# Kernel optimization log

Hardware: AMD Instinct MI355X
Metric: run time of the kernel (lower is better)

Reference implementation:

```python
import jax, jax.numpy as jnp
import numpy as np


def setup_inputs() -> dict:
    key = jax.random.key(0)
    ks = jax.random.split(key, 9)
    b, t_q, t_k, n_q, n_k = 4, 128, 512, 512, 512
    out_size = 512
    s = 0.02  # small init scale for weights
    return {
        "query": jax.random.normal(ks[0], (b, t_q, n_q), jnp.float32),
        "keys": jax.random.normal(ks[1], (b, t_k, n_k), jnp.float32),
        "values": jax.random.normal(ks[2], (b, t_k, n_k), jnp.float32),
        "W_q": jax.random.normal(ks[3], (n_k, n_q), jnp.float32) * s,
        "b_q": jnp.zeros((n_k,), jnp.float32),
        "w_att": jax.random.normal(ks[4], (n_k,), jnp.float32) * s,
        "b_att": jnp.zeros((1,), jnp.float32),
        "W_out": jax.random.normal(ks[5], (out_size, n_q + n_k), jnp.float32) * s,
        "b_out": jnp.zeros((out_size,), jnp.float32),
    }


def reference(query, keys, values, W_q, b_q, w_att, b_att, W_out, b_out):
    # linear_q: [b, t_q, query_size] -> [b, t_q, key_size]
    att_query = jnp.einsum("bqd,nd->bqn", query, W_q) + b_q
    # Bahdanau additive score: tanh(q + k) projected by linear_att (key_size -> 1)
    # intermediate: [b, t_q, t_k, n]
    sum_qk = jnp.tanh(att_query[:, :, None, :] + keys[:, None, :, :])
    scores = jnp.einsum("bqkn,n->bqk", sum_qk, w_att) + b_att[0]
    # mask is None by default; dropout p=0 -> identity
    probs = jax.nn.softmax(scores, axis=-1)  # [b, t_q, t_k]
    context = jnp.einsum("bqk,bkn->bqn", probs, values)
    # linear_out on concat([query, context]) + tanh nonlinearity
    cat = jnp.concatenate([query, context], axis=-1)
    out = jnp.tanh(jnp.einsum("bqc,oc->bqo", cat, W_out) + b_out)
    return out, probs
```

## Files before the change

### kernel.cpp

```cpp
#include <hip/hip_runtime.h>
#include <hip/hip_fp16.h>


#define BB    4
#define TQ    128
#define TK    512
#define NN    512
#define OUTSZ 512
#define CATSZ 1024
#define K2E   2.8853900817779268f
#define L2E   1.4426950408889634f
#define MAT   262144
#define WS_HALVES (11 * MAT)

typedef __attribute__((ext_vector_type(4))) _Float16 half4;
typedef __attribute__((ext_vector_type(2))) _Float16 h2;

#if __has_builtin(__builtin_amdgcn_exp2f)
#define EXP2F(x) __builtin_amdgcn_exp2f(x)
#else
#define EXP2F(x) exp2f(x)
#endif
#if __has_builtin(__builtin_amdgcn_rcpf)
#define RCPF(x) __builtin_amdgcn_rcpf(x)
#else
#define RCPF(x) (1.0f / (x))
#endif

__device__ __forceinline__ h2 u2h(unsigned int u) {
  union { unsigned int i; h2 h; } v; v.i = u; return v.h;
}
#if __has_builtin(__builtin_amdgcn_fdot2)
__device__ __forceinline__ float FDOT2(h2 a, h2 b, float c) {
  return __builtin_amdgcn_fdot2(a, b, c, false);
}
#else
__device__ __forceinline__ float FDOT2(h2 a, h2 b, float c) {
  return fmaf((float)a.x, (float)b.x, fmaf((float)a.y, (float)b.y, c));
}
#endif

__device__ __forceinline__ float fast_tanh(float x) {
  float e = EXP2F(x * K2E);
  return fmaf(-2.0f, RCPF(e + 1.0f), 1.0f);
}
__device__ __forceinline__ float waveRedSum(float s) {
  #pragma unroll
  for (int m = 32; m >= 1; m >>= 1) s += __shfl_xor(s, m, 64);
  return s;
}
__device__ __forceinline__ float waveRedMax(float s) {
  #pragma unroll
  for (int m = 32; m >= 1; m >>= 1) s = fmaxf(s, __shfl_xor(s, m, 64));
  return s;
}
__device__ __forceinline__ float fma4(float4 w, float4 v, float acc) {
  acc = fmaf(w.x, v.x, acc); acc = fmaf(w.y, v.y, acc);
  acc = fmaf(w.z, v.z, acc); acc = fmaf(w.w, v.w, acc);
  return acc;
}
__device__ __forceinline__ float4 scqh(float4 s, half4 E, float A, float w) {
  s.x = fmaf(w, RCPF(fmaf((float)E.x, A, 1.0f)), s.x);
  s.y = fmaf(w, RCPF(fmaf((float)E.y, A, 1.0f)), s.y);
  s.z = fmaf(w, RCPF(fmaf((float)E.z, A, 1.0f)), s.z);
  s.w = fmaf(w, RCPF(fmaf((float)E.w, A, 1.0f)), s.w);
  return s;
}
__device__ __forceinline__ void dotq(float4& r0, float4& r1, uint4 wp, uint2 cp) {
  h2 c0 = u2h(cp.x), c1 = u2h(cp.y);
  r0.x = FDOT2(u2h(wp.x), c0, r0.x); r1.x = FDOT2(u2h(wp.x), c1, r1.x);
  r0.y = FDOT2(u2h(wp.y), c0, r0.y); r1.y = FDOT2(u2h(wp.y), c1, r1.y);
  r0.z = FDOT2(u2h(wp.z), c0, r0.z); r1.z = FDOT2(u2h(wp.z), c1, r1.z);
  r0.w = FDOT2(u2h(wp.w), c0, r0.w); r1.w = FDOT2(u2h(wp.w), c1, r1.w);
}

__global__ __launch_bounds__(256)
void pack_kernel(const float* __restrict__ keys, const float* __restrict__ W_q,
                 const float* __restrict__ W_out, const float* __restrict__ values,
                 _Float16* __restrict__ ws)
{
  __shared__ float tile[32][33];
  const int idx = blockIdx.x;
  const int tx = threadIdx.x & 31, ty = threadIdx.x >> 5;

  if (idx >= 1792) {
    int r = idx - 1792;
    int b = r >> 8, k2 = r & 255;
    const float* r0 = values + ((size_t)b * 512 + 2 * k2) * 512;
    const float* r1 = r0 + 512;
    int n0 = threadIdx.x * 2;
    float2 a = *(const float2*)(r0 + n0);
    float2 c = *(const float2*)(r1 + n0);
    _Float16* dst = ws + (size_t)7 * MAT + (size_t)b * MAT + k2 * 1024 + n0 * 2;
    half4 h = {(_Float16)a.x, (_Float16)c.x, (_Float16)a.y, (_Float16)c.y};
    *(half4*)dst = h;
    return;
  }

  if (idx < 1024) {
    int b = idx >> 8, r = idx & 255;
    int by = r >> 4, bx = r & 15;
    const float* src = keys + (size_t)b * MAT;
    _Float16* dst = ws + (size_t)b * MAT;
    #pragma unroll
    for (int i = 0; i < 32; i += 8)
      tile[ty + i][tx] = src[(size_t)(by * 32 + ty + i) * 512 + bx * 32 + tx] * K2E;
    __syncthreads();
    #pragma unroll
    for (int i = 0; i < 32; i += 8)
      dst[(size_t)(bx * 32 + ty + i) * 512 + by * 32 + tx] = (_Float16)EXP2F(tile[tx][ty + i]);
    return;
  }

  const float* src; _Float16* dst; int N; int by, bx;
  if (idx < 1280) {
    int r = idx - 1024; by = r >> 4; bx = r & 15;
    src = W_q; dst = ws + (size_t)4 * MAT; N = 512;
  } else {
    int r = idx - 1280; by = r >> 5; bx = r & 31;
    src = W_out; dst = ws + (size_t)5 * MAT; N = 1024;
  }
  #pragma unroll
  for (int i = 0; i < 32; i += 8)
    tile[ty + i][tx] = src[(size_t)(by * 32 + ty + i) * N + bx * 32 + tx];
  __syncthreads();
  #pragma unroll
  for (int i = 0; i < 32; i += 8) {
    int d = bx * 32 + ty + i;
    int o = by * 32 + tx;
    dst[(size_t)(d >> 1) * 1024 + o * 2 + (d & 1)] = (_Float16)tile[tx][ty + i];
  }
}

__global__ __launch_bounds__(1024, 4)
void attn_main(const float* __restrict__ query,
               const float* __restrict__ b_q, const float* __restrict__ w_att,
               const float* __restrict__ b_att, const float* __restrict__ b_out,
               const _Float16* __restrict__ ws,
               float* __restrict__ out, float* __restrict__ probs)
{
  __shared__ __align__(16) _Float16 catH[2048];
  __shared__ __align__(16) float4 paw[NN];
  __shared__ __align__(16) _Float16 prH[1024];
  __shared__ __align__(16) float  pt[8][2][NN];
  __shared__ float redm[2][8], reds2[2][8], redw[8];

  const _Float16* wsKeys  = ws;
  const _Float16* wsWqP   = ws + (size_t)4 * MAT;
  const _Float16* wsWoutP = ws + (size_t)5 * MAT;
  const _Float16* wsValP  = ws + (size_t)7 * MAT;

  const int t    = threadIdx.x;
  const int qh   = t >> 9;
  const int u    = t & 511;
  const int G    = t >> 7;
  const int v    = t & 127;
  const int wave = t >> 6, lane = t & 63, wq8 = wave & 7;

  const int p  = blockIdx.x;
  const int b  = (p & 7) >> 1;
  const int qg = ((p >> 3) << 1) | (p & 1);
  const int qabs0 = qg * 2;

  const float batt = b_att[0];

  float w_own = 0.f;
  if (qh == 0) {
    float q0 = query[((size_t)(b * TQ + qabs0 + 0)) * NN + u];
    float q1 = query[((size_t)(b * TQ + qabs0 + 1)) * NN + u];
    catH[(u >> 1) * 4 + (u & 1)]     = (_Float16)q0;
    catH[(u >> 1) * 4 + 2 + (u & 1)] = (_Float16)q1;
  } else {
    w_own = w_att[u];
  }
  if (qh == 1) {
    float wp = waveRedSum(w_own);
    if (lane == 0) redw[wq8] = wp;
  }
  __syncthreads();
  const float sumW = redw[0]+redw[1]+redw[2]+redw[3]+redw[4]+redw[5]+redw[6]+redw[7];

  {
    const _Float16* wq = wsWqP + 8 * v;
    float4 a0 = {0,0,0,0}, a1 = {0,0,0,0};
    #pragma unroll 4
    for (int j2 = 0; j2 < 32; ++j2) {
      int d2 = 32 * G + j2;
      uint4 wp = *(const uint4*)(wq + (size_t)d2 * 1024);
      uint2 cp = *(const uint2*)(&catH[d2 * 4]);
      dotq(a0, a1, wp, cp);
    }
    *(float4*)(&pt[G][0][4 * v]) = a0;
    *(float4*)(&pt[G][1][4 * v]) = a1;
  }
  __syncthreads();
  {
    float s = pt[0][qh][u] + pt[1][qh][u] + pt[2][qh][u] + pt[3][qh][u]
            + pt[4][qh][u] + pt[5][qh][u] + pt[6][qh][u] + pt[7][qh][u];
    float A = EXP2F(K2E * (s + b_q[u]));
    if (qh == 0) { paw[u].x = A; paw[u].z = w_att[u]; }
    else         { paw[u].y = A; }
  }
  __syncthreads();

  {
    const _Float16* ke = wsKeys + (size_t)b * MAT + 4 * v;
    float4 s0 = {0,0,0,0}, s1 = {0,0,0,0};
    #pragma unroll 8
    for (int j = 0; j < 64; ++j) {
      int n = 64 * G + j;
      half4 E   = *(const half4*)(ke + (size_t)n * 512);
      float4 pw = paw[n];
      s0 = scqh(s0, E, pw.x, pw.z);
      s1 = scqh(s1, E, pw.y, pw.z);
    }
    *(float4*)(&pt[G][0][4 * v]) = s0;
    *(float4*)(&pt[G][1][4 * v]) = s1;
  }
  __syncthreads();

  {
    float s = pt[0][qh][u] + pt[1][qh][u] + pt[2][qh][u] + pt[3][qh][u]
            + pt[4][qh][u] + pt[5][qh][u] + pt[6][qh][u] + pt[7][qh][u];
    float sc = batt + sumW - 2.0f * s;
    float m = waveRedMax(sc);
    if (lane == 0) redm[qh][wq8] = m;
    __syncthreads();
    float bm = fmaxf(fmaxf(fmaxf(redm[qh][0],redm[qh][1]),fmaxf(redm[qh][2],redm[qh][3])),
                     fmaxf(fmaxf(redm[qh][4],redm[qh][5]),fmaxf(redm[qh][6],redm[qh][7])));
    float e = EXP2F((sc - bm) * L2E);
    float se = waveRedSum(e);
    if (lane == 0) reds2[qh][wq8] = se;
    __syncthreads();
    float bs = reds2[qh][0]+reds2[qh][1]+reds2[qh][2]+reds2[qh][3]
             + reds2[qh][4]+reds2[qh][5]+reds2[qh][6]+reds2[qh][7];
    float pv = e * RCPF(bs);
    prH[(u >> 1) * 4 + qh * 2 + (u & 1)] = (_Float16)pv;
    probs[((size_t)(b * TQ + qabs0 + qh)) * TK + u] = pv;
  }
  __syncthreads();

  {
    const _Float16* vp = wsValP + (size_t)b * MAT + 8 * v;
    float4 c0 = {0,0,0,0}, c1 = {0,0,0,0};
    #pragma unroll 4
    for (int j2 = 0; j2 < 32; ++j2) {
      int k2 = 32 * G + j2;
      uint4 vk = *(const uint4*)(vp + (size_t)k2 * 1024);
      uint2 pp = *(const uint2*)(&prH[k2 * 4]);
      dotq(c0, c1, vk, pp);
    }
    *(float4*)(&pt[G][0][4 * v]) = c0;
    *(float4*)(&pt[G][1][4 * v]) = c1;
  }
  __syncthreads();
  {
    float s = pt[0][qh][u] + pt[1][qh][u] + pt[2][qh][u] + pt[3][qh][u]
            + pt[4][qh][u] + pt[5][qh][u] + pt[6][qh][u] + pt[7][qh][u];
    catH[(256 + (u >> 1)) * 4 + qh * 2 + (u & 1)] = (_Float16)s;
  }
  __syncthreads();

  {
    const _Float16* wo = wsWoutP + 8 * v;
    float4 o0 = {0,0,0,0}, o1 = {0,0,0,0};
    #pragma unroll 4
    for (int j2 = 0; j2 < 64; ++j2) {
      int c2 = 64 * G + j2;
      uint4 wp = *(const uint4*)(wo + (size_t)c2 * 1024);
      uint2 cp = *(const uint2*)(&catH[c2 * 4]);
      dotq(o0, o1, wp, cp);
    }
    *(float4*)(&pt[G][0][4 * v]) = o0;
    *(float4*)(&pt[G][1][4 * v]) = o1;
  }
  __syncthreads();
  {
    float s = pt[0][qh][u] + pt[1][qh][u] + pt[2][qh][u] + pt[3][qh][u]
            + pt[4][qh][u] + pt[5][qh][u] + pt[6][qh][u] + pt[7][qh][u];
    float oo = s + b_out[u];
    out[((size_t)(b * TQ + qabs0 + qh)) * OUTSZ + u] = fast_tanh(oo);
  }
}

__device__ __forceinline__ float sc4f(float4 w, float4 k, float4 a, float acc) {
  acc = fmaf(w.x, RCPF(EXP2F(fmaf(k.x, K2E, a.x)) + 1.0f), acc);
  acc = fmaf(w.y, RCPF(EXP2F(fmaf(k.y, K2E, a.y)) + 1.0f), acc);
  acc = fmaf(w.z, RCPF(EXP2F(fmaf(k.z, K2E, a.z)) + 1.0f), acc);
  acc = fmaf(w.w, RCPF(EXP2F(fmaf(k.w, K2E, a.w)) + 1.0f), acc);
  return acc;
}

__global__ __launch_bounds__(1024, 4)
void attn_fallback(const float* __restrict__ query, const float* __restrict__ keys,
                   const float* __restrict__ values, const float* __restrict__ W_q,
                   const float* __restrict__ b_q, const float* __restrict__ w_att,
                   const float* __restrict__ b_att, const float* __restrict__ W_out,
                   const float* __restrict__ b_out,
                   float* __restrict__ out, float* __restrict__ probs)
{
  __shared__ __align__(16) float qv[2][NN];
  __shared__ __align__(16) float aqc[2][NN];
  __shared__ __align__(16) float wv[NN];
  __shared__ __align__(16) float pr[2][TK];
  __shared__ __align__(16) float ctx[2][NN];
  __shared__ __align__(16) float part[2][2][NN];
  __shared__ float redm[2][8], reds[2][8], redw[8];

  const int t = threadIdx.x, H = t >> 9, u = t & 511;
  const int wave = t >> 6, lane = t & 63, wq8 = wave & 7;
  const int p = blockIdx.x, b = (p & 7) >> 1;
  const int qg = ((p >> 3) << 1) | (p & 1), qabs0 = qg * 2;
  const float batt = b_att[0];

  if (H == 0) wv[u] = w_att[u];
  qv[H][u] = query[((size_t)(b * TQ + qabs0 + H)) * NN + u];
  __syncthreads();
  if (H == 0) {
    float wp = waveRedSum(wv[u]);
    if (lane == 0) redw[wq8] = wp;
  }
  __syncthreads();
  const float sumW = redw[0]+redw[1]+redw[2]+redw[3]+redw[4]+redw[5]+redw[6]+redw[7];

  {
    const float4* wq4 = (const float4*)(W_q + (size_t)u * NN + 256 * H);
    const float4* x4  = (const float4*)(qv[0] + 256 * H);
    const float4* y4  = (const float4*)(qv[1] + 256 * H);
    float a0=0.f, a0b=0.f, a1=0.f, a1b=0.f;
    #pragma unroll 2
    for (int c = 0; c < 16; ++c) {
      float4 wA=wq4[4*c+0], wB=wq4[4*c+1], wC=wq4[4*c+2], wD=wq4[4*c+3];
      float4 xA=x4[4*c+0], xB=x4[4*c+1], xC=x4[4*c+2], xD=x4[4*c+3];
      a0 = fma4(wA,xA,a0); a0b = fma4(wB,xB,a0b);
      a0 = fma4(wC,xC,a0); a0b = fma4(wD,xD,a0b);
      float4 yA=y4[4*c+0], yB=y4[4*c+1], yC=y4[4*c+2], yD=y4[4*c+3];
      a1 = fma4(wA,yA,a1); a1b = fma4(wB,yB,a1b);
      a1 = fma4(wC,yC,a1); a1b = fma4(wD,yD,a1b);
    }
    part[H][0][u] = a0 + a0b; part[H][1][u] = a1 + a1b;
  }
  __syncthreads();
  aqc[H][u] = (part[0][H][u] + part[1][H][u] + b_q[u]) * K2E;
  __syncthreads();

  {
    const float4* kr  = (const float4*)(keys + ((size_t)(b * TK) + u) * NN + 256 * H);
    const float4* a0p = (const float4*)(aqc[0] + 256 * H);
    const float4* a1p = (const float4*)(aqc[1] + 256 * H);
    const float4* w4  = (const float4*)(wv + 256 * H);
    float s0 = 0.f, s1 = 0.f;
    #pragma unroll 2
    for (int c = 0; c < 16; ++c) {
      float4 kA=kr[4*c+0], kB=kr[4*c+1], kC=kr[4*c+2], kD=kr[4*c+3];
      float4 wA=w4[4*c+0], wB=w4[4*c+1], wC=w4[4*c+2], wD=w4[4*c+3];
      float4 aA=a0p[4*c+0], aB=a0p[4*c+1], aC=a0p[4*c+2], aD=a0p[4*c+3];
      s0 = sc4f(wA,kA,aA,s0); s0 = sc4f(wB,kB,aB,s0);
      s0 = sc4f(wC,kC,aC,s0); s0 = sc4f(wD,kD,aD,s0);
      float4 bA=a1p[4*c+0], bB=a1p[4*c+1], bC=a1p[4*c+2], bD=a1p[4*c+3];
      s1 = sc4f(wA,kA,bA,s1); s1 = sc4f(wB,kB,bB,s1);
      s1 = sc4f(wC,kC,bC,s1); s1 = sc4f(wD,kD,bD,s1);
    }
    part[H][0][u] = s0; part[H][1][u] = s1;
  }
  __syncthreads();

  {
    float sc = batt + sumW - 2.0f * (part[0][H][u] + part[1][H][u]);
    float m = waveRedMax(sc);
    if (lane == 0) redm[H][wq8] = m;
    __syncthreads();
    float bm = fmaxf(fmaxf(fmaxf(redm[H][0],redm[H][1]),fmaxf(redm[H][2],redm[H][3])),
                     fmaxf(fmaxf(redm[H][4],redm[H][5]),fmaxf(redm[H][6],redm[H][7])));
    float e = EXP2F((sc - bm) * L2E);
    float se = waveRedSum(e);
    if (lane == 0) reds[H][wq8] = se;
    __syncthreads();
    float bs = reds[H][0]+reds[H][1]+reds[H][2]+reds[H][3]
             + reds[H][4]+reds[H][5]+reds[H][6]+reds[H][7];
    float pv = e * RCPF(bs);
    pr[H][u] = pv;
    probs[((size_t)(b * TQ + qabs0 + H)) * TK + u] = pv;
  }
  __syncthreads();

  {
    const float* vcol = values + ((size_t)(b * TK) + 256 * H) * NN + u;
    const float4* p0 = (const float4*)(pr[0] + 256 * H);
    const float4* p1 = (const float4*)(pr[1] + 256 * H);
    float c0a=0.f, c0b=0.f, c1a=0.f, c1b=0.f;
    #pragma unroll 2
    for (int k = 0; k < 256; k += 8) {
      float v0 = vcol[(size_t)(k+0)*NN]; float v1 = vcol[(size_t)(k+1)*NN];
      float v2 = vcol[(size_t)(k+2)*NN]; float v3 = vcol[(size_t)(k+3)*NN];
      float v4 = vcol[(size_t)(k+4)*NN]; float v5 = vcol[(size_t)(k+5)*NN];
      float v6 = vcol[(size_t)(k+6)*NN]; float v7 = vcol[(size_t)(k+7)*NN];
      float4 pA = p0[k>>2], pB = p0[(k>>2)+1];
      float4 qA = p1[k>>2], qB = p1[(k>>2)+1];
      c0a = fmaf(pA.x,v0,c0a); c0a = fmaf(pA.y,v1,c0a);
      c0b = fmaf(pA.z,v2,c0b); c0b = fmaf(pA.w,v3,c0b);
      c0a = fmaf(pB.x,v4,c0a); c0a = fmaf(pB.y,v5,c0a);
      c0b = fmaf(pB.z,v6,c0b); c0b = fmaf(pB.w,v7,c0b);
      c1a = fmaf(qA.x,v0,c1a); c1a = fmaf(qA.y,v1,c1a);
      c1b = fmaf(qA.z,v2,c1b); c1b = fmaf(qA.w,v3,c1b);
      c1a = fmaf(qB.x,v4,c1a); c1a = fmaf(qB.y,v5,c1a);
      c1b = fmaf(qB.z,v6,c1b); c1b = fmaf(qB.w,v7,c1b);
    }
    part[H][0][u] = c0a + c0b; part[H][1][u] = c1a + c1b;
  }
  __syncthreads();
  ctx[H][u] = part[0][H][u] + part[1][H][u];
  __syncthreads();

  {
    const float4* wo = (const float4*)(W_out + (size_t)u * CATSZ + 512 * H);
    const float4* x4 = (H == 0) ? (const float4*)qv[0] : (const float4*)ctx[0];
    const float4* y4 = (H == 0) ? (const float4*)qv[1] : (const float4*)ctx[1];
    float o0=0.f, o0b=0.f, o1=0.f, o1b=0.f;
    #pragma unroll 2
    for (int c = 0; c < 32; ++c) {
      float4 wA=wo[4*c+0], wB=wo[4*c+1], wC=wo[4*c+2], wD=wo[4*c+3];
      float4 xA=x4[4*c+0], xB=x4[4*c+1], xC=x4[4*c+2], xD=x4[4*c+3];
      o0 = fma4(wA,xA,o0); o0b = fma4(wB,xB,o0b);
      o0 = fma4(wC,xC,o0); o0b = fma4(wD,xD,o0b);
      float4 yA=y4[4*c+0], yB=y4[4*c+1], yC=y4[4*c+2], yD=y4[4*c+3];
      o1 = fma4(wA,yA,o1); o1b = fma4(wB,yB,o1b);
      o1 = fma4(wC,yC,o1); o1b = fma4(wD,yD,o1b);
    }
    part[H][0][u] = o0 + o0b; part[H][1][u] = o1 + o1b;
  }
  __syncthreads();
  {
    float oo = part[0][H][u] + part[1][H][u] + b_out[u];
    out[((size_t)(b * TQ + qabs0 + H)) * OUTSZ + u] = fast_tanh(oo);
  }
}

extern "C" void kernel_launch(void* const* d_in, const int* in_sizes, int n_in,
                              void* d_out, int out_size, void* d_ws, size_t ws_size,
                              hipStream_t stream) {
  const float* query = (const float*)d_in[0];
  const float* keys  = (const float*)d_in[1];
  const float* vals  = (const float*)d_in[2];
  const float* W_q   = (const float*)d_in[3];
  const float* b_q   = (const float*)d_in[4];
  const float* w_att = (const float*)d_in[5];
  const float* b_att = (const float*)d_in[6];
  const float* W_out = (const float*)d_in[7];
  const float* b_out = (const float*)d_in[8];

  float* out   = (float*)d_out;
  float* probs = out + (size_t)BB * TQ * OUTSZ;

  if (ws_size >= (size_t)WS_HALVES * sizeof(_Float16)) {
    _Float16* ws = (_Float16*)d_ws;
    pack_kernel<<<dim3(2816), dim3(256), 0, stream>>>(keys, W_q, W_out, vals, ws);
    attn_main<<<dim3(BB * TQ / 2), dim3(1024), 0, stream>>>(
        query, b_q, w_att, b_att, b_out, ws, out, probs);
  } else {
    attn_fallback<<<dim3(BB * TQ / 2), dim3(1024), 0, stream>>>(
        query, keys, vals, W_q, b_q, w_att, b_att, W_out, b_out, out, probs);
  }
}
```

Baseline: 117.3 us.

## Drop softmax max pass and constant terms; widen key loads and store partials as half

Measured after the change: 119.0 us. Within noise of the previous version (+1.4%).

```diff
diff --git a/kernel.cpp b/kernel.cpp
--- a/kernel.cpp
+++ b/kernel.cpp
@@ -47,11 +47,6 @@
 __device__ __forceinline__ float waveRedSum(float s) {
   #pragma unroll
   for (int m = 32; m >= 1; m >>= 1) s += __shfl_xor(s, m, 64);
-  return s;
-}
-__device__ __forceinline__ float waveRedMax(float s) {
-  #pragma unroll
-  for (int m = 32; m >= 1; m >>= 1) s = fmaxf(s, __shfl_xor(s, m, 64));
   return s;
 }
 __device__ __forceinline__ float fma4(float4 w, float4 v, float acc) {
@@ -143,7 +138,9 @@
   __shared__ __align__(16) float4 paw[NN];
   __shared__ __align__(16) _Float16 prH[1024];
   __shared__ __align__(16) float  pt[8][2][NN];
-  __shared__ float redm[2][8], reds2[2][8], redw[8];
+  __shared__ float reds2[2][8], redw[8];
+
+  _Float16* ptH = (_Float16*)pt;
 
   const _Float16* wsKeys  = ws;
   const _Float16* wsWqP   = ws + (size_t)4 * MAT;
@@ -155,6 +152,8 @@
   const int u    = t & 511;
   const int G    = t >> 7;
   const int v    = t & 127;
+  const int G16  = t >> 6;
+  const int v6   = t & 63;
   const int wave = t >> 6, lane = t & 63, wq8 = wave & 7;
 
   const int p  = blockIdx.x;
@@ -162,23 +161,13 @@
   const int qg = ((p >> 3) << 1) | (p & 1);
   const int qabs0 = qg * 2;
 
-  const float batt = b_att[0];
-
-  float w_own = 0.f;
   if (qh == 0) {
     float q0 = query[((size_t)(b * TQ + qabs0 + 0)) * NN + u];
     float q1 = query[((size_t)(b * TQ + qabs0 + 1)) * NN + u];
     catH[(u >> 1) * 4 + (u & 1)]     = (_Float16)q0;
     catH[(u >> 1) * 4 + 2 + (u & 1)] = (_Float16)q1;
-  } else {
-    w_own = w_att[u];
-  }
-  if (qh == 1) {
-    float wp = waveRedSum(w_own);
-    if (lane == 0) redw[wq8] = wp;
-  }
-  __syncthreads();
-  const float sumW = redw[0]+redw[1]+redw[2]+redw[3]+redw[4]+redw[5]+redw[6]+redw[7];
+  }
+  __syncthreads();
 
   {
     const _Float16* wq = wsWqP + 8 * v;
@@ -204,31 +193,46 @@
   __syncthreads();
 
   {
-    const _Float16* ke = wsKeys + (size_t)b * MAT + 4 * v;
-    float4 s0 = {0,0,0,0}, s1 = {0,0,0,0};
-    #pragma unroll 8
-    for (int j = 0; j < 64; ++j) {
-      int n = 64 * G + j;
-      half4 E   = *(const half4*)(ke + (size_t)n * 512);
+    const _Float16* ke = wsKeys + (size_t)b * MAT + 8 * v6;
+    float4 s0a = {0,0,0,0}, s0b = {0,0,0,0};
+    float4 s1a = {0,0,0,0}, s1b = {0,0,0,0};
+    #pragma unroll 4
+    for (int j = 0; j < 32; ++j) {
+      int n = 32 * G16 + j;
+      uint4 Eu = *(const uint4*)(ke + (size_t)n * 512);
+      half4 Elo; { union { uint2 u; half4 h; } c; c.u = make_uint2(Eu.x, Eu.y); Elo = c.h; }
+      half4 Ehi; { union { uint2 u; half4 h; } c; c.u = make_uint2(Eu.z, Eu.w); Ehi = c.h; }
       float4 pw = paw[n];
-      s0 = scqh(s0, E, pw.x, pw.z);
-      s1 = scqh(s1, E, pw.y, pw.z);
-    }
-    *(float4*)(&pt[G][0][4 * v]) = s0;
-    *(float4*)(&pt[G][1][4 * v]) = s1;
-  }
-  __syncthreads();
-
-  {
-    float s = pt[0][qh][u] + pt[1][qh][u] + pt[2][qh][u] + pt[3][qh][u]
-            + pt[4][qh][u] + pt[5][qh][u] + pt[6][qh][u] + pt[7][qh][u];
-    float sc = batt + sumW - 2.0f * s;
-    float m = waveRedMax(sc);
-    if (lane == 0) redm[qh][wq8] = m;
-    __syncthreads();
-    float bm = fmaxf(fmaxf(fmaxf(redm[qh][0],redm[qh][1]),fmaxf(redm[qh][2],redm[qh][3])),
-                     fmaxf(fmaxf(redm[qh][4],redm[qh][5]),fmaxf(redm[qh][6],redm[qh][7])));
-    float e = EXP2F((sc - bm) * L2E);
+      s0a = scqh(s0a, Elo, pw.x, pw.z);
+      s0b = scqh(s0b, Ehi, pw.x, pw.z);
+      s1a = scqh(s1a, Elo, pw.y, pw.z);
+      s1b = scqh(s1b, Ehi, pw.y, pw.z);
+    }
+    int base0 = (8 * v6) * 16 + G16;
+    ptH[base0 +   0] = (_Float16)s0a.x; ptH[base0 +  16] = (_Float16)s0a.y;
+    ptH[base0 +  32] = (_Float16)s0a.z; ptH[base0 +  48] = (_Float16)s0a.w;
+    ptH[base0 +  64] = (_Float16)s0b.x; ptH[base0 +  80] = (_Float16)s0b.y;
+    ptH[base0 +  96] = (_Float16)s0b.z; ptH[base0 + 112] = (_Float16)s0b.w;
+    int base1 = 8192 + base0;
+    ptH[base1 +   0] = (_Float16)s1a.x; ptH[base1 +  16] = (_Float16)s1a.y;
+    ptH[base1 +  32] = (_Float16)s1a.z; ptH[base1 +  48] = (_Float16)s1a.w;
+    ptH[base1 +  64] = (_Float16)s1b.x; ptH[base1 +  80] = (_Float16)s1b.y;
+    ptH[base1 +  96] = (_Float16)s1b.z; ptH[base1 + 112] = (_Float16)s1b.w;
+  }
+  __syncthreads();
+
+  {
+    const _Float16* pp = ptH + qh * 8192 + u * 16;
+    uint4 h0 = *(const uint4*)(pp);
+    uint4 h1 = *(const uint4*)(pp + 8);
+    unsigned int packs[8] = {h0.x, h0.y, h0.z, h0.w, h1.x, h1.y, h1.z, h1.w};
+    float s = 0.f;
+    #pragma unroll
+    for (int i = 0; i < 8; ++i) {
+      h2 a = u2h(packs[i]);
+      s += (float)a.x + (float)a.y;
+    }
+    float e = EXP2F(-K2E * s);
     float se = waveRedSum(e);
     if (lane == 0) reds2[qh][wq8] = se;
     __syncthreads();
@@ -367,7 +371,9 @@
 
   {
     float sc = batt + sumW - 2.0f * (part[0][H][u] + part[1][H][u]);
-    float m = waveRedMax(sc);
+    float m = sc;
+    #pragma unroll
+    for (int mm = 32; mm >= 1; mm >>= 1) m = fmaxf(m, __shfl_xor(m, mm, 64));
     if (lane == 0) redm[H][wq8] = m;
     __syncthreads();
     float bm = fmaxf(fmaxf(fmaxf(redm[H][0],redm[H][1]),fmaxf(redm[H][2],redm[H][3])),
```
